# Kernel tuning notes

Measured on AMD Instinct MI355X. Metric: run time of the kernel, lower is better.

Reference implementation:

```python
import jax, jax.numpy as jnp
import numpy as np

DIM, HEAD, FFN = 256, 4, 1024
NEG = -1e9


def layer_norm(x, g, b, eps=1e-5):
    mu = jnp.mean(x, axis=-1, keepdims=True)
    var = jnp.mean((x - mu) ** 2, axis=-1, keepdims=True)
    return (x - mu) / jnp.sqrt(var + eps) * g + b


def setup_inputs() -> dict:
    key = jax.random.key(0)
    ks = jax.random.split(key, 10)
    B, T, D = 8, 2048, DIM
    s = 1.0 / np.sqrt(D)
    x = jax.random.normal(ks[0], (B, T, D), dtype=jnp.float32)
    mask = jax.random.randint(ks[1], (B, T), 0, 2).astype(jnp.float32)
    Wqkv = jax.random.uniform(ks[2], (3 * D, D), jnp.float32, -s, s)
    bqkv = jnp.zeros((3 * D,), jnp.float32)
    Wo = jax.random.uniform(ks[3], (D, D), jnp.float32, -s, s)
    bo = jnp.zeros((D,), jnp.float32)
    W1 = jax.random.uniform(ks[4], (FFN, D), jnp.float32, -s, s)
    b1 = jnp.zeros((FFN,), jnp.float32)
    W2 = jax.random.uniform(ks[5], (D, FFN), jnp.float32, -1.0 / np.sqrt(FFN), 1.0 / np.sqrt(FFN))
    b2 = jnp.zeros((D,), jnp.float32)
    g1 = jnp.ones((D,), jnp.float32); be1 = jnp.zeros((D,), jnp.float32)
    g2 = jnp.ones((D,), jnp.float32); be2 = jnp.zeros((D,), jnp.float32)
    return dict(x=x, mask=mask, Wqkv=Wqkv, bqkv=bqkv, Wo=Wo, bo=bo,
                W1=W1, b1=b1, W2=W2, b2=b2, g1=g1, be1=be1, g2=g2, be2=be2)


def _forward(x, mask, Wqkv, bqkv, Wo, bo, W1, b1, W2, b2, g1, be1, g2, be2):
    B, T, D = x.shape
    H = HEAD
    hd = D // H
    # --- MultiheadAttention (explicit, non-flash path, need_weights=True) ---
    qkv = jnp.einsum('btd,ed->bte', x, Wqkv) + bqkv            # (B,T,3D)
    q, k, v = jnp.split(qkv, 3, axis=-1)
    q = q.reshape(B, T, H, hd).transpose(0, 2, 1, 3)           # (B,H,T,hd)
    k = k.reshape(B, T, H, hd).transpose(0, 2, 1, 3)
    v = v.reshape(B, T, H, hd).transpose(0, 2, 1, 3)
    scores = jnp.einsum('bhqd,bhkd->bhqk', q, k) / jnp.sqrt(jnp.float32(hd))
    scores = jnp.where(mask[:, None, None, :] > 0.5, NEG, scores)
    w = jax.nn.softmax(scores, axis=-1)                        # (B,H,T,T)
    attn = jnp.einsum('bhqk,bhkd->bhqd', w, v)                 # (B,H,T,hd)
    attn = attn.transpose(0, 2, 1, 3).reshape(B, T, D)
    attn_out = jnp.einsum('btd,ed->bte', attn, Wo) + bo        # (B,T,D)
    w_avg = jnp.mean(w, axis=1)                                # (B,T,T), averaged over heads
    # halting score: sum over query dim (dim=1), then masked softmax
    halting = jnp.sum(w_avg, axis=1)                           # (B,T)
    halting = jax.nn.softmax(halting + mask * (-1e10), axis=-1)
    # --- residual + LN + FFN + LN ---
    h = layer_norm(x + attn_out, g1, be1)
    ffn = jnp.einsum('btf,df->btd', jax.nn.relu(jnp.einsum('btd,fd->btf', h, W1) + b1), W2) + b2
    out = layer_norm(h + ffn, g2, be2)
    return out, halting


def reference(x, mask, Wqkv, bqkv, Wo, bo, W1, b1, W2, b2, g1, be1, g2, be2):
    return _forward(x, mask, Wqkv, bqkv, Wo, bo, W1, b1, W2, b2, g1, be1, g2, be2)
```

## Files before the change

kernel.cpp:

```cpp
#include <hip/hip_runtime.h>
#include <hip/hip_bf16.h>
#include <math.h>

namespace {

constexpr int B = 8, T = 2048, D = 256, H = 4, HD = 64, FF = 1024;
constexpr float QSCALE = 0.18033688f;

typedef __attribute__((ext_vector_type(8))) short short8;
typedef __attribute__((ext_vector_type(4))) short s16x4;
typedef __attribute__((ext_vector_type(4))) float f32x4;

__device__ __forceinline__ float dot4(float4 a, float4 b) {
    return a.x*b.x + a.y*b.y + a.z*b.z + a.w*b.w;
}
__device__ __forceinline__ short f2bf(float f) {
    __hip_bfloat16 h = __float2bfloat16(f);
    return *reinterpret_cast<short*>(&h);
}
__device__ __forceinline__ float exp2a(float x) {
    float r; asm("v_exp_f32 %0, %1" : "=v"(r) : "v"(x)); return r;
}
__device__ __forceinline__ unsigned cvtpk(float lo, float hi) {
    unsigned r; asm("v_cvt_pk_bf16_f32 %0, %1, %2" : "=v"(r) : "v"(lo), "v"(hi)); return r;
}

__global__ __launch_bounds__(256) void k_cvt(
        const float* __restrict__ x,  const float* __restrict__ wq,
        const float* __restrict__ wo, const float* __restrict__ w1,
        const float* __restrict__ w2,
        short* __restrict__ x16,  short* __restrict__ wq16,
        short* __restrict__ wo16, short* __restrict__ w116,
        short* __restrict__ w216) {
    const int N0 = 524288, N1 = 24576, N2 = 8192, N3 = 32768, N4 = 32768;
    const int total = N0 + N1 + N2 + N3 + N4;
    for (int i = blockIdx.x*256 + threadIdx.x; i < total; i += gridDim.x*256) {
        const float* s; short* d; int j = i;
        if (j < N0) { s = x; d = x16; }
        else { j -= N0;
            if (j < N1) { s = wq; d = wq16; }
            else { j -= N1;
                if (j < N2) { s = wo; d = wo16; }
                else { j -= N2;
                    if (j < N3) { s = w1; d = w116; }
                    else { j -= N3; s = w2; d = w216; }
                }
            }
        }
        float4 a = ((const float4*)s)[j*2], b2 = ((const float4*)s)[j*2+1];
        short8 o;
        o[0]=f2bf(a.x);  o[1]=f2bf(a.y);  o[2]=f2bf(a.z);  o[3]=f2bf(a.w);
        o[4]=f2bf(b2.x); o[5]=f2bf(b2.y); o[6]=f2bf(b2.z); o[7]=f2bf(b2.w);
        ((short8*)d)[j] = o;
    }
}

template<int MODE>
__global__ __launch_bounds__(256) void k_gemm(
        const short* __restrict__ A, const short* __restrict__ W,
        const float* __restrict__ bias, const int K,
        short* __restrict__ oq, short* __restrict__ ok, short* __restrict__ ov,
        float* __restrict__ of, short* __restrict__ o16) {
    __shared__ short As[64][72];
    __shared__ short Ws[64][72];
    __shared__ float Cs[64][68];
    const int tid = threadIdx.x;
    const int w = tid >> 6, lane = tid & 63;
    const int qr = lane & 15, g = lane >> 4;
    const int wm = w >> 1, wn = w & 1;
    const int m0 = blockIdx.x * 64;
    const int n0 = blockIdx.y * 64;
    const int srow = tid >> 2, scol = (tid & 3) * 8;
    const short* Ag = A + (size_t)(m0 + srow) * K + scol;
    const short* Wg = W + (size_t)(n0 + srow) * K + scol;

    f32x4 acc[2][2];
    #pragma unroll
    for (int i = 0; i < 2; i++)
        #pragma unroll
        for (int j = 0; j < 2; j++) acc[i][j] = (f32x4){0.f, 0.f, 0.f, 0.f};

    for (int k0 = 0; k0 < K; k0 += 64) {
        __syncthreads();
        *(short8*)&As[srow][scol]      = *(const short8*)(Ag + k0);
        *(short8*)&As[srow][scol + 32] = *(const short8*)(Ag + k0 + 32);
        *(short8*)&Ws[srow][scol]      = *(const short8*)(Wg + k0);
        *(short8*)&Ws[srow][scol + 32] = *(const short8*)(Wg + k0 + 32);
        __syncthreads();
        #pragma unroll
        for (int kk = 0; kk < 2; kk++) {
            short8 a0 = *(const short8*)&As[wm*32 + qr][g*8 + kk*32];
            short8 a1 = *(const short8*)&As[wm*32 + 16 + qr][g*8 + kk*32];
            short8 b0 = *(const short8*)&Ws[wn*32 + qr][g*8 + kk*32];
            short8 b1 = *(const short8*)&Ws[wn*32 + 16 + qr][g*8 + kk*32];
            acc[0][0] = __builtin_amdgcn_mfma_f32_16x16x32_bf16(a0, b0, acc[0][0], 0, 0, 0);
            acc[0][1] = __builtin_amdgcn_mfma_f32_16x16x32_bf16(a0, b1, acc[0][1], 0, 0, 0);
            acc[1][0] = __builtin_amdgcn_mfma_f32_16x16x32_bf16(a1, b0, acc[1][0], 0, 0, 0);
            acc[1][1] = __builtin_amdgcn_mfma_f32_16x16x32_bf16(a1, b1, acc[1][1], 0, 0, 0);
        }
    }

    const int b = m0 >> 11;
    const int tl0 = m0 & (T - 1);

    if (MODE == 0 && blockIdx.y >= 8) {
        const int h = (int)blockIdx.y - 8;
        #pragma unroll
        for (int fm = 0; fm < 2; fm++) {
            const int tbase = tl0 + wm*32 + fm*16 + g*4;
            #pragma unroll
            for (int fn = 0; fn < 2; fn++) {
                const int d = wn*32 + fn*16 + qr;
                const float bv = bias[n0 + d];
                s16x4 pk;
                #pragma unroll
                for (int r = 0; r < 4; r++) pk[r] = f2bf(acc[fm][fn][r] + bv);
                *(s16x4*)&ov[((size_t)(b*H + h)*HD + d)*T + tbase] = pk;
            }
        }
        return;
    }

    #pragma unroll
    for (int fm = 0; fm < 2; fm++)
        #pragma unroll
        for (int fn = 0; fn < 2; fn++)
            #pragma unroll
            for (int r = 0; r < 4; r++)
                Cs[wm*32 + fm*16 + g*4 + r][wn*32 + fn*16 + qr] = acc[fm][fn][r];
    __syncthreads();
    const int row = tid >> 2, c0 = (tid & 3) * 16;
    float vals[16];
    #pragma unroll
    for (int j = 0; j < 16; j++) vals[j] = Cs[row][c0 + j] + bias[n0 + c0 + j];

    if (MODE == 0) {
        const int by = blockIdx.y;
        short* dst = (by < 4) ? oq : ok;
        const float qs = (by < 4) ? QSCALE : 1.0f;
        const int h = by & 3;
        short8 s0, s1;
        #pragma unroll
        for (int j = 0; j < 8; j++) { s0[j] = f2bf(vals[j]*qs); s1[j] = f2bf(vals[8+j]*qs); }
        short* p = dst + ((size_t)(b*H + h)*T + tl0 + row)*HD + c0;
        *(short8*)p = s0;
        *(short8*)(p + 8) = s1;
    } else if (MODE == 1 || MODE == 3) {
        float* p = of + (size_t)(m0 + row)*256 + n0 + c0;
        #pragma unroll
        for (int jj = 0; jj < 4; jj++) *(float4*)(p + jj*4) = *(float4*)&vals[jj*4];
    } else {
        short8 s0, s1;
        #pragma unroll
        for (int j = 0; j < 8; j++) {
            s0[j] = f2bf(fmaxf(vals[j], 0.f));
            s1[j] = f2bf(fmaxf(vals[8+j], 0.f));
        }
        short* p = o16 + (size_t)(m0 + row)*1024 + n0 + c0;
        *(short8*)p = s0;
        *(short8*)(p + 8) = s1;
    }
}

__global__ __launch_bounds__(256) void k_flash(
        const short* __restrict__ qb, const short* __restrict__ kb,
        const short* __restrict__ vtb, const float* __restrict__ mask,
        short* __restrict__ attnb, float* __restrict__ part) {
    __shared__ short Ks[64][72];
    __shared__ short Vt[64][72];
    __shared__ short Ps[4][16][72];
    __shared__ float msk[64];
    __shared__ float colacc[4][64];

    const int tid = threadIdx.x;
    const int w = tid >> 6, lane = tid & 63;
    const int qr = lane & 15, g = lane >> 4;
    const int qt = blockIdx.x, h = blockIdx.y, b = blockIdx.z;
    const int bh = b*H + h;
    const int q0 = qt*64 + w*16;

    const short* qg = qb + ((size_t)bh * T + q0) * HD;
    const short8 qf0 = *(const short8*)(qg + qr*HD + g*8);
    const short8 qf1 = *(const short8*)(qg + qr*HD + 32 + g*8);

    const short* kg0 = kb + (size_t)bh * T * HD;
    const short* vg0 = vtb + (size_t)bh * HD * T;
    const float* mg  = mask + (size_t)b * T;
    const int skey = tid >> 2, sc = tid & 3;

    float lrun = 0.f;
    f32x4 oa[4];
    #pragma unroll
    for (int i = 0; i < 4; i++) oa[i] = (f32x4){0.f, 0.f, 0.f, 0.f};

    for (int kt = 0; kt < T/64; kt++) {
        __syncthreads();
        {
            const short* kg = kg0 + (size_t)(kt*64) * HD;
            *(short8*)&Ks[skey][sc*8]      = *(const short8*)(kg + skey*HD + sc*8);
            *(short8*)&Ks[skey][sc*8 + 32] = *(const short8*)(kg + skey*HD + sc*8 + 32);
            const short* vg = vg0 + kt*64;
            *(short8*)&Vt[skey][sc*8]      = *(const short8*)(vg + (size_t)skey*T + sc*8);
            *(short8*)&Vt[skey][sc*8 + 32] = *(const short8*)(vg + (size_t)skey*T + sc*8 + 32);
            if (tid < 64) msk[tid] = mg[kt*64 + tid];
        }
        __syncthreads();

        float p[4][4];
        float lsum = 0.f;
        #pragma unroll
        for (int t4 = 0; t4 < 4; t4++) {
            f32x4 sa = (f32x4){0.f, 0.f, 0.f, 0.f};
            short8 kf0 = *(const short8*)&Ks[t4*16 + qr][g*8];
            short8 kf1 = *(const short8*)&Ks[t4*16 + qr][g*8 + 32];
            sa = __builtin_amdgcn_mfma_f32_16x16x32_bf16(kf0, qf0, sa, 0, 0, 0);
            sa = __builtin_amdgcn_mfma_f32_16x16x32_bf16(kf1, qf1, sa, 0, 0, 0);
            const float4 mv4 = *(const float4*)&msk[t4*16 + 4*g];
            p[t4][0] = (mv4.x > 0.5f) ? 0.f : exp2a(sa[0]);
            p[t4][1] = (mv4.y > 0.5f) ? 0.f : exp2a(sa[1]);
            p[t4][2] = (mv4.z > 0.5f) ? 0.f : exp2a(sa[2]);
            p[t4][3] = (mv4.w > 0.5f) ? 0.f : exp2a(sa[3]);
            lsum += (p[t4][0] + p[t4][1]) + (p[t4][2] + p[t4][3]);
        }
        lsum += __shfl_xor(lsum, 16, 64);
        lsum += __shfl_xor(lsum, 32, 64);
        lrun += lsum;

        #pragma unroll
        for (int t4 = 0; t4 < 4; t4++) {
            union { unsigned u[2]; s16x4 s; } cv;
            cv.u[0] = cvtpk(p[t4][0], p[t4][1]);
            cv.u[1] = cvtpk(p[t4][2], p[t4][3]);
            *(s16x4*)&Ps[w][qr][t4*16 + 4*g] = cv.s;
        }
        asm volatile("" ::: "memory");
        const short8 pa0 = *(const short8*)&Ps[w][qr][g*8];
        const short8 pa1 = *(const short8*)&Ps[w][qr][g*8 + 32];

        #pragma unroll
        for (int nt = 0; nt < 4; nt++) {
            short8 vf0 = *(const short8*)&Vt[nt*16 + qr][g*8];
            short8 vf1 = *(const short8*)&Vt[nt*16 + qr][g*8 + 32];
            oa[nt] = __builtin_amdgcn_mfma_f32_16x16x32_bf16(vf0, pa0, oa[nt], 0, 0, 0);
            oa[nt] = __builtin_amdgcn_mfma_f32_16x16x32_bf16(vf1, pa1, oa[nt], 0, 0, 0);
        }
    }

    const float invl = 1.f / lrun;
    #pragma unroll
    for (int nt = 0; nt < 4; nt++) {
        s16x4 pk;
        #pragma unroll
        for (int r = 0; r < 4; r++) pk[r] = f2bf(oa[nt][r] * invl);
        *(s16x4*)&attnb[((size_t)b*T + q0 + qr)*D + h*HD + nt*16 + 4*g] = pk;
    }
    float linv_r[4];
    #pragma unroll
    for (int r = 0; r < 4; r++) linv_r[r] = __shfl(invl, 4*g + r, 64);

    for (int kt = 0; kt < T/64; kt++) {
        __syncthreads();
        {
            const short* kg = kg0 + (size_t)(kt*64) * HD;
            *(short8*)&Ks[skey][sc*8]      = *(const short8*)(kg + skey*HD + sc*8);
            *(short8*)&Ks[skey][sc*8 + 32] = *(const short8*)(kg + skey*HD + sc*8 + 32);
            if (tid < 64) msk[tid] = mg[kt*64 + tid];
        }
        __syncthreads();
        float cs[4];
        #pragma unroll
        for (int t4 = 0; t4 < 4; t4++) {
            f32x4 sa = (f32x4){0.f, 0.f, 0.f, 0.f};
            short8 kf0 = *(const short8*)&Ks[t4*16 + qr][g*8];
            short8 kf1 = *(const short8*)&Ks[t4*16 + qr][g*8 + 32];
            sa = __builtin_amdgcn_mfma_f32_16x16x32_bf16(qf0, kf0, sa, 0, 0, 0);
            sa = __builtin_amdgcn_mfma_f32_16x16x32_bf16(qf1, kf1, sa, 0, 0, 0);
            float c = exp2a(sa[0])*linv_r[0] + exp2a(sa[1])*linv_r[1]
                    + exp2a(sa[2])*linv_r[2] + exp2a(sa[3])*linv_r[3];
            cs[t4] = (msk[t4*16 + qr] > 0.5f) ? 0.f : c;
        }
        #pragma unroll
        for (int t4 = 0; t4 < 4; t4++) {
            cs[t4] += __shfl_xor(cs[t4], 16, 64);
            cs[t4] += __shfl_xor(cs[t4], 32, 64);
        }
        if (lane < 16) {
            #pragma unroll
            for (int t4 = 0; t4 < 4; t4++) colacc[w][t4*16 + lane] = cs[t4];
        }
        __syncthreads();
        if (tid < 64)
            part[((size_t)bh*32 + qt)*T + kt*64 + tid] =
                colacc[0][tid] + colacc[1][tid] + colacc[2][tid] + colacc[3][tid];
    }
}

__global__ __launch_bounds__(256) void k_red(
        const float* __restrict__ part, float* __restrict__ red) {
    __shared__ float s[128];
    const int b = blockIdx.y, kc = blockIdx.x;
    const int tid = threadIdx.x;
    const int c = tid & 127, half = tid >> 7;
    const int k = kc*128 + c;
    const float* pb = part + ((size_t)(b*128 + half*64))*T + k;
    float acc = 0.f;
    #pragma unroll 8
    for (int r = 0; r < 64; r++) acc += pb[(size_t)r*T];
    if (half) s[c] = acc;
    __syncthreads();
    if (!half) red[(size_t)b*T + k] = acc + s[c];
}

__global__ __launch_bounds__(256) void k_halt(
        const float* __restrict__ red, const float* __restrict__ mask,
        float* __restrict__ outh) {
    __shared__ float redm[4], reds[4];
    const int b = blockIdx.x, tid = threadIdx.x;
    const float* mg = mask + (size_t)b * T;
    float v[8];
    float M = -3e38f;
    #pragma unroll
    for (int i = 0; i < 8; i++) {
        v[i] = red[(size_t)b*T + tid + i*256]*0.25f + mg[tid + i*256]*(-1e10f);
        M = fmaxf(M, v[i]);
    }
    #pragma unroll
    for (int off = 1; off < 64; off <<= 1) M = fmaxf(M, __shfl_xor(M, off, 64));
    const int wv = tid >> 6, lane = tid & 63;
    if (lane == 0) redm[wv] = M;
    __syncthreads();
    M = fmaxf(fmaxf(redm[0], redm[1]), fmaxf(redm[2], redm[3]));
    float S = 0.f;
    #pragma unroll
    for (int i = 0; i < 8; i++) { v[i] = __expf(v[i] - M); S += v[i]; }
    #pragma unroll
    for (int off = 1; off < 64; off <<= 1) S += __shfl_xor(S, off, 64);
    if (lane == 0) reds[wv] = S;
    __syncthreads();
    const float invS = 1.f / (reds[0] + reds[1] + reds[2] + reds[3]);
    #pragma unroll
    for (int i = 0; i < 8; i++) outh[(size_t)b*T + tid + i*256] = v[i]*invS;
}

__global__ __launch_bounds__(256) void k_ln(
        const float* __restrict__ a, const float* __restrict__ bsrc,
        const float* __restrict__ g, const float* __restrict__ be,
        float* __restrict__ yf, short* __restrict__ y16) {
    __shared__ float s[16][D];
    const int tid = threadIdx.x;
    const size_t row0 = (size_t)blockIdx.x * 16;
    const float4* ag = (const float4*)(a + row0*D);
    const float4* bg = (const float4*)(bsrc + row0*D);
    #pragma unroll
    for (int i = 0; i < 4; i++) {
        float4 av = ag[tid + i*256], bv = bg[tid + i*256];
        float4 sv = {av.x+bv.x, av.y+bv.y, av.z+bv.z, av.w+bv.w};
        ((float4*)&s[0][0])[tid + i*256] = sv;
    }
    __syncthreads();
    const int wv = tid >> 6, lane = tid & 63;
    float gvv[4], bvv[4];
    #pragma unroll
    for (int s2 = 0; s2 < 4; s2++) { gvv[s2] = g[lane + 64*s2]; bvv[s2] = be[lane + 64*s2]; }
    #pragma unroll
    for (int rr = 0; rr < 4; rr++) {
        const int r = wv*4 + rr;
        float x0 = s[r][lane],     x1 = s[r][lane+64];
        float x2 = s[r][lane+128], x3 = s[r][lane+192];
        float sum = x0+x1+x2+x3;
        float ssq = x0*x0 + x1*x1 + x2*x2 + x3*x3;
        #pragma unroll
        for (int off = 1; off < 64; off <<= 1) {
            sum += __shfl_xor(sum, off, 64);
            ssq += __shfl_xor(ssq, off, 64);
        }
        const float mu = sum * (1.f/256.f);
        const float rs = rsqrtf(ssq*(1.f/256.f) - mu*mu + 1e-5f);
        float y0 = (x0 - mu)*rs*gvv[0] + bvv[0];
        float y1 = (x1 - mu)*rs*gvv[1] + bvv[1];
        float y2 = (x2 - mu)*rs*gvv[2] + bvv[2];
        float y3 = (x3 - mu)*rs*gvv[3] + bvv[3];
        float* yp = yf + (row0 + r)*D;
        yp[lane]     = y0;
        yp[lane+64]  = y1;
        yp[lane+128] = y2;
        yp[lane+192] = y3;
        if (y16) {
            short* hp = y16 + (row0 + r)*D;
            hp[lane]     = f2bf(y0);
            hp[lane+64]  = f2bf(y1);
            hp[lane+128] = f2bf(y2);
            hp[lane+192] = f2bf(y3);
        }
    }
}

}

extern "C" void kernel_launch(void* const* d_in, const int* in_sizes, int n_in,
                              void* d_out, int out_size, void* d_ws, size_t ws_size,
                              hipStream_t stream) {
    (void)in_sizes; (void)n_in; (void)out_size; (void)ws_size;
    const float* x    = (const float*)d_in[0];
    const float* mask = (const float*)d_in[1];
    const float* Wqkv = (const float*)d_in[2];
    const float* bqkv = (const float*)d_in[3];
    const float* Wo   = (const float*)d_in[4];
    const float* bo   = (const float*)d_in[5];
    const float* W1   = (const float*)d_in[6];
    const float* b1   = (const float*)d_in[7];
    const float* W2   = (const float*)d_in[8];
    const float* b2   = (const float*)d_in[9];
    const float* g1   = (const float*)d_in[10];
    const float* be1  = (const float*)d_in[11];
    const float* g2   = (const float*)d_in[12];
    const float* be2  = (const float*)d_in[13];

    float* out  = (float*)d_out;
    char*  wsb  = (char*)d_ws;
    const size_t MB = 1024*1024;

    short* qb16   = (short*)(wsb + 0*MB);
    short* kb16   = (short*)(wsb + 8*MB);
    short* vt16   = (short*)(wsb + 16*MB);
    short* x16    = (short*)(wsb + 24*MB);
    short* attn16 = (short*)(wsb + 24*MB);
    float* part   = (float*)(wsb + 32*MB);
    float* hb     = (float*)(wsb + 40*MB);
    short* h16    = (short*)(wsb + 56*MB);
    short* wq16   = (short*)(wsb + 64*MB);
    short* wo16   = (short*)(wsb + 64*MB + 393216);
    short* w116   = (short*)(wsb + 64*MB + 524288);
    short* w216   = (short*)(wsb + 64*MB + 1048576);
    float* po     = (float*)(wsb + 66*MB);
    float* fo     = (float*)(wsb + 66*MB);
    short* mid16  = (short*)(wsb + 0*MB);
    float* redb   = (float*)(wsb + 82*MB);
    float* outh   = out + (size_t)B*T*D;

    k_cvt    <<<dim3(1024),        256, 0, stream>>>(x, Wqkv, Wo, W1, W2,
                                                     x16, wq16, wo16, w116, w216);
    k_gemm<0><<<dim3(256, 12),     256, 0, stream>>>(x16, wq16, bqkv, 256,
                                                     qb16, kb16, vt16, nullptr, nullptr);
    k_flash  <<<dim3(T/64, H, B),  256, 0, stream>>>(qb16, kb16, vt16, mask, attn16, part);
    k_red    <<<dim3(16, B),       256, 0, stream>>>(part, redb);
    k_halt   <<<dim3(B),           256, 0, stream>>>(redb, mask, outh);
    k_gemm<1><<<dim3(256, 4),      256, 0, stream>>>(attn16, wo16, bo, 256,
                                                     nullptr, nullptr, nullptr, po, nullptr);
    k_ln     <<<dim3(B*T/16),      256, 0, stream>>>(x, po, g1, be1, hb, h16);
    k_gemm<2><<<dim3(256, 16),     256, 0, stream>>>(h16, w116, b1, 256,
                                                     nullptr, nullptr, nullptr, nullptr, mid16);
    k_gemm<3><<<dim3(256, 4),      256, 0, stream>>>(mid16, w216, b2, 1024,
                                                     nullptr, nullptr, nullptr, fo, nullptr);
    k_ln     <<<dim3(B*T/16),      256, 0, stream>>>(hb, fo, g2, be2, out, nullptr);
}
```

Baseline: 241.3 us.

## Split attention kernel into key-split passes with a combine kernel

```diff
diff --git a/kernel.cpp b/kernel.cpp
--- a/kernel.cpp
+++ b/kernel.cpp
@@ -11,12 +11,14 @@
 typedef __attribute__((ext_vector_type(4))) short s16x4;
 typedef __attribute__((ext_vector_type(4))) float f32x4;
 
-__device__ __forceinline__ float dot4(float4 a, float4 b) {
-    return a.x*b.x + a.y*b.y + a.z*b.z + a.w*b.w;
-}
 __device__ __forceinline__ short f2bf(float f) {
     __hip_bfloat16 h = __float2bfloat16(f);
     return *reinterpret_cast<short*>(&h);
+}
+__device__ __forceinline__ float bf2f(short s) {
+    union { unsigned u; float f; } c;
+    c.u = ((unsigned)(unsigned short)s) << 16;
+    return c.f;
 }
 __device__ __forceinline__ float exp2a(float x) {
     float r; asm("v_exp_f32 %0, %1" : "=v"(r) : "v"(x)); return r;
@@ -162,20 +164,20 @@
     }
 }
 
-__global__ __launch_bounds__(256) void k_flash(
+__global__ __launch_bounds__(256) void k_flash1(
         const short* __restrict__ qb, const short* __restrict__ kb,
         const short* __restrict__ vtb, const float* __restrict__ mask,
-        short* __restrict__ attnb, float* __restrict__ part) {
+        short* __restrict__ opart, float* __restrict__ lpart) {
     __shared__ short Ks[64][72];
     __shared__ short Vt[64][72];
     __shared__ short Ps[4][16][72];
-    __shared__ float msk[64];
-    __shared__ float colacc[4][64];
+    __shared__ float mskb[64];
 
     const int tid = threadIdx.x;
     const int w = tid >> 6, lane = tid & 63;
     const int qr = lane & 15, g = lane >> 4;
-    const int qt = blockIdx.x, h = blockIdx.y, b = blockIdx.z;
+    const int kh = blockIdx.x & 1, qt = blockIdx.x >> 1;
+    const int h = blockIdx.y, b = blockIdx.z;
     const int bh = b*H + h;
     const int q0 = qt*64 + w*16;
 
@@ -183,9 +185,9 @@
     const short8 qf0 = *(const short8*)(qg + qr*HD + g*8);
     const short8 qf1 = *(const short8*)(qg + qr*HD + 32 + g*8);
 
-    const short* kg0 = kb + (size_t)bh * T * HD;
-    const short* vg0 = vtb + (size_t)bh * HD * T;
-    const float* mg  = mask + (size_t)b * T;
+    const short* kg0 = kb + (size_t)bh * T * HD + (size_t)kh * 1024 * HD;
+    const short* vg0 = vtb + (size_t)bh * HD * T + kh * 1024;
+    const float* mg  = mask + (size_t)b * T + kh * 1024;
     const int skey = tid >> 2, sc = tid & 3;
 
     float lrun = 0.f;
@@ -193,7 +195,7 @@
     #pragma unroll
     for (int i = 0; i < 4; i++) oa[i] = (f32x4){0.f, 0.f, 0.f, 0.f};
 
-    for (int kt = 0; kt < T/64; kt++) {
+    for (int kt = 0; kt < 16; kt++) {
         __syncthreads();
         {
             const short* kg = kg0 + (size_t)(kt*64) * HD;
@@ -202,7 +204,7 @@
             const short* vg = vg0 + kt*64;
             *(short8*)&Vt[skey][sc*8]      = *(const short8*)(vg + (size_t)skey*T + sc*8);
             *(short8*)&Vt[skey][sc*8 + 32] = *(const short8*)(vg + (size_t)skey*T + sc*8 + 32);
-            if (tid < 64) msk[tid] = mg[kt*64 + tid];
+            if (tid < 64) mskb[tid] = (mg[kt*64 + tid] > 0.5f) ? -1e9f : 0.f;
         }
         __syncthreads();
 
@@ -210,16 +212,16 @@
         float lsum = 0.f;
         #pragma unroll
         for (int t4 = 0; t4 < 4; t4++) {
-            f32x4 sa = (f32x4){0.f, 0.f, 0.f, 0.f};
+            const float4 mb4 = *(const float4*)&mskb[t4*16 + 4*g];
+            f32x4 sa = (f32x4){mb4.x, mb4.y, mb4.z, mb4.w};
             short8 kf0 = *(const short8*)&Ks[t4*16 + qr][g*8];
             short8 kf1 = *(const short8*)&Ks[t4*16 + qr][g*8 + 32];
             sa = __builtin_amdgcn_mfma_f32_16x16x32_bf16(kf0, qf0, sa, 0, 0, 0);
             sa = __builtin_amdgcn_mfma_f32_16x16x32_bf16(kf1, qf1, sa, 0, 0, 0);
-            const float4 mv4 = *(const float4*)&msk[t4*16 + 4*g];
-            p[t4][0] = (mv4.x > 0.5f) ? 0.f : exp2a(sa[0]);
-            p[t4][1] = (mv4.y > 0.5f) ? 0.f : exp2a(sa[1]);
-            p[t4][2] = (mv4.z > 0.5f) ? 0.f : exp2a(sa[2]);
-            p[t4][3] = (mv4.w > 0.5f) ? 0.f : exp2a(sa[3]);
+            p[t4][0] = exp2a(sa[0]);
+            p[t4][1] = exp2a(sa[1]);
+            p[t4][2] = exp2a(sa[2]);
+            p[t4][3] = exp2a(sa[3]);
             lsum += (p[t4][0] + p[t4][1]) + (p[t4][2] + p[t4][3]);
         }
         lsum += __shfl_xor(lsum, 16, 64);
@@ -246,38 +248,86 @@
         }
     }
 
-    const float invl = 1.f / lrun;
+    const size_t obase = ((size_t)(kh*32 + bh)*2048 + q0 + qr) * 64;
     #pragma unroll
     for (int nt = 0; nt < 4; nt++) {
         s16x4 pk;
         #pragma unroll
-        for (int r = 0; r < 4; r++) pk[r] = f2bf(oa[nt][r] * invl);
-        *(s16x4*)&attnb[((size_t)b*T + q0 + qr)*D + h*HD + nt*16 + 4*g] = pk;
-    }
-    float linv_r[4];
-    #pragma unroll
-    for (int r = 0; r < 4; r++) linv_r[r] = __shfl(invl, 4*g + r, 64);
-
-    for (int kt = 0; kt < T/64; kt++) {
+        for (int r = 0; r < 4; r++) pk[r] = f2bf(oa[nt][r]);
+        *(s16x4*)&opart[obase + nt*16 + 4*g] = pk;
+    }
+    if (lane < 16)
+        lpart[(size_t)(kh*32 + bh)*2048 + q0 + qr] = lrun;
+}
+
+__global__ __launch_bounds__(256) void k_comb(
+        const short* __restrict__ opart, const float* __restrict__ lpart,
+        short* __restrict__ attnb, float* __restrict__ invlb) {
+    const int j = blockIdx.x*256 + threadIdx.x;
+    const size_t flat = (size_t)j * 8;
+    const int d0 = (int)(flat & 63);
+    const int q  = (int)((flat >> 6) & 2047);
+    const int bh = (int)(flat >> 17);
+    short8 o0 = *(const short8*)&opart[flat];
+    short8 o1 = *(const short8*)&opart[flat + (size_t)4194304];
+    const float l = lpart[bh*2048 + q] + lpart[65536 + bh*2048 + q];
+    const float inv = 1.f / l;
+    short8 r;
+    #pragma unroll
+    for (int i = 0; i < 8; i++) r[i] = f2bf((bf2f(o0[i]) + bf2f(o1[i])) * inv);
+    const int b = bh >> 2, h = bh & 3;
+    *(short8*)&attnb[((size_t)(b*2048 + q))*256 + h*64 + d0] = r;
+    if (d0 == 0) invlb[bh*2048 + q] = inv;
+}
+
+__global__ __launch_bounds__(256) void k_flash2(
+        const short* __restrict__ qb, const short* __restrict__ kb,
+        const float* __restrict__ mask, const float* __restrict__ invlb,
+        float* __restrict__ part) {
+    __shared__ short Ks[64][72];
+    __shared__ float mskb[64];
+    __shared__ float colacc[4][64];
+
+    const int tid = threadIdx.x;
+    const int w = tid >> 6, lane = tid & 63;
+    const int qr = lane & 15, g = lane >> 4;
+    const int kh = blockIdx.x & 1, qt = blockIdx.x >> 1;
+    const int h = blockIdx.y, b = blockIdx.z;
+    const int bh = b*H + h;
+    const int q0 = qt*64 + w*16;
+
+    const short* qg = qb + ((size_t)bh * T + q0) * HD;
+    const short8 qf0 = *(const short8*)(qg + qr*HD + g*8);
+    const short8 qf1 = *(const short8*)(qg + qr*HD + 32 + g*8);
+
+    float linv[4];
+    #pragma unroll
+    for (int r = 0; r < 4; r++) linv[r] = invlb[bh*2048 + q0 + 4*g + r];
+
+    const short* kg0 = kb + (size_t)bh * T * HD + (size_t)kh * 1024 * HD;
+    const float* mg  = mask + (size_t)b * T + kh * 1024;
+    const int skey = tid >> 2, sc = tid & 3;
+
+    for (int kt = 0; kt < 16; kt++) {
         __syncthreads();
         {
             const short* kg = kg0 + (size_t)(kt*64) * HD;
             *(short8*)&Ks[skey][sc*8]      = *(const short8*)(kg + skey*HD + sc*8);
             *(short8*)&Ks[skey][sc*8 + 32] = *(const short8*)(kg + skey*HD + sc*8 + 32);
-            if (tid < 64) msk[tid] = mg[kt*64 + tid];
+            if (tid < 64) mskb[tid] = (mg[kt*64 + tid] > 0.5f) ? -1e9f : 0.f;
         }
         __syncthreads();
         float cs[4];
         #pragma unroll
         for (int t4 = 0; t4 < 4; t4++) {
-            f32x4 sa = (f32x4){0.f, 0.f, 0.f, 0.f};
+            const float mb = mskb[t4*16 + qr];
+            f32x4 sa = (f32x4){mb, mb, mb, mb};
             short8 kf0 = *(const short8*)&Ks[t4*16 + qr][g*8];
             short8 kf1 = *(const short8*)&Ks[t4*16 + qr][g*8 + 32];
             sa = __builtin_amdgcn_mfma_f32_16x16x32_bf16(qf0, kf0, sa, 0, 0, 0);
             sa = __builtin_amdgcn_mfma_f32_16x16x32_bf16(qf1, kf1, sa, 0, 0, 0);
-            float c = exp2a(sa[0])*linv_r[0] + exp2a(sa[1])*linv_r[1]
-                    + exp2a(sa[2])*linv_r[2] + exp2a(sa[3])*linv_r[3];
-            cs[t4] = (msk[t4*16 + qr] > 0.5f) ? 0.f : c;
+            cs[t4] = exp2a(sa[0])*linv[0] + exp2a(sa[1])*linv[1]
+                   + exp2a(sa[2])*linv[2] + exp2a(sa[3])*linv[3];
         }
         #pragma unroll
         for (int t4 = 0; t4 < 4; t4++) {
@@ -290,7 +340,7 @@
         }
         __syncthreads();
         if (tid < 64)
-            part[((size_t)bh*32 + qt)*T + kt*64 + tid] =
+            part[((size_t)bh*32 + qt)*T + kh*1024 + kt*64 + tid] =
                 colacc[0][tid] + colacc[1][tid] + colacc[2][tid] + colacc[3][tid];
     }
 }
@@ -425,24 +475,29 @@
     short* vt16   = (short*)(wsb + 16*MB);
     short* x16    = (short*)(wsb + 24*MB);
     short* attn16 = (short*)(wsb + 24*MB);
+    short* opart  = (short*)(wsb + 32*MB);
     float* part   = (float*)(wsb + 32*MB);
-    float* hb     = (float*)(wsb + 40*MB);
-    short* h16    = (short*)(wsb + 56*MB);
-    short* wq16   = (short*)(wsb + 64*MB);
-    short* wo16   = (short*)(wsb + 64*MB + 393216);
-    short* w116   = (short*)(wsb + 64*MB + 524288);
-    short* w216   = (short*)(wsb + 64*MB + 1048576);
-    float* po     = (float*)(wsb + 66*MB);
-    float* fo     = (float*)(wsb + 66*MB);
+    float* redb   = (float*)(wsb + 40*MB);
+    float* hb     = (float*)(wsb + 48*MB);
+    short* h16    = (short*)(wsb + 64*MB);
+    float* lpart  = (float*)(wsb + 72*MB);
+    float* invlb  = (float*)(wsb + 72*MB + 524288);
+    short* wq16   = (short*)(wsb + 73*MB);
+    short* wo16   = (short*)(wsb + 73*MB + 393216);
+    short* w116   = (short*)(wsb + 73*MB + 524288);
+    short* w216   = (short*)(wsb + 73*MB + 1048576);
+    float* po     = (float*)(wsb + 75*MB);
+    float* fo     = (float*)(wsb + 75*MB);
     short* mid16  = (short*)(wsb + 0*MB);
-    float* redb   = (float*)(wsb + 82*MB);
     float* outh   = out + (size_t)B*T*D;
 
     k_cvt    <<<dim3(1024),        256, 0, stream>>>(x, Wqkv, Wo, W1, W2,
                                                      x16, wq16, wo16, w116, w216);
     k_gemm<0><<<dim3(256, 12),     256, 0, stream>>>(x16, wq16, bqkv, 256,
                                                      qb16, kb16, vt16, nullptr, nullptr);
-    k_flash  <<<dim3(T/64, H, B),  256, 0, stream>>>(qb16, kb16, vt16, mask, attn16, part);
+    k_flash1 <<<dim3(64, H, B),    256, 0, stream>>>(qb16, kb16, vt16, mask, opart, lpart);
+    k_comb   <<<dim3(2048),        256, 0, stream>>>(opart, lpart, attn16, invlb);
+    k_flash2 <<<dim3(64, H, B),    256, 0, stream>>>(qb16, kb16, mask, invlb, part);
     k_red    <<<dim3(16, B),       256, 0, stream>>>(part, redb);
     k_halt   <<<dim3(B),           256, 0, stream>>>(redb, mask, outh);
     k_gemm<1><<<dim3(256, 4),      256, 0, stream>>>(attn16, wo16, bo, 256,
```

Result: no change. 237.6 us (-1.5%).

## Split flash attention into row-sum pass and fused normalized attention with column sums

Applied to the files above, without the earlier changes.

```diff
diff --git a/kernel.cpp b/kernel.cpp
--- a/kernel.cpp
+++ b/kernel.cpp
@@ -11,9 +11,6 @@
 typedef __attribute__((ext_vector_type(4))) short s16x4;
 typedef __attribute__((ext_vector_type(4))) float f32x4;
 
-__device__ __forceinline__ float dot4(float4 a, float4 b) {
-    return a.x*b.x + a.y*b.y + a.z*b.z + a.w*b.w;
-}
 __device__ __forceinline__ short f2bf(float f) {
     __hip_bfloat16 h = __float2bfloat16(f);
     return *reinterpret_cast<short*>(&h);
@@ -162,136 +159,227 @@
     }
 }
 
-__global__ __launch_bounds__(256) void k_flash(
+__global__ __launch_bounds__(256) void k_flashL(
         const short* __restrict__ qb, const short* __restrict__ kb,
-        const short* __restrict__ vtb, const float* __restrict__ mask,
-        short* __restrict__ attnb, float* __restrict__ part) {
-    __shared__ short Ks[64][72];
-    __shared__ short Vt[64][72];
-    __shared__ short Ps[4][16][72];
-    __shared__ float msk[64];
-    __shared__ float colacc[4][64];
-
+        const float* __restrict__ mask, float* __restrict__ liout) {
+    __shared__ short Ks[128][72];
+    __shared__ float lbuf[4][4][16];
     const int tid = threadIdx.x;
     const int w = tid >> 6, lane = tid & 63;
     const int qr = lane & 15, g = lane >> 4;
     const int qt = blockIdx.x, h = blockIdx.y, b = blockIdx.z;
     const int bh = b*H + h;
-    const int q0 = qt*64 + w*16;
-
-    const short* qg = qb + ((size_t)bh * T + q0) * HD;
-    const short8 qf0 = *(const short8*)(qg + qr*HD + g*8);
-    const short8 qf1 = *(const short8*)(qg + qr*HD + 32 + g*8);
-
+    const int q0 = qt*64;
+
+    short8 qf[4][2];
+    {
+        const short* qg = qb + ((size_t)bh * T + q0) * HD;
+        #pragma unroll
+        for (int qt4 = 0; qt4 < 4; qt4++) {
+            qf[qt4][0] = *(const short8*)(qg + (qt4*16 + qr)*HD + g*8);
+            qf[qt4][1] = *(const short8*)(qg + (qt4*16 + qr)*HD + 32 + g*8);
+        }
+    }
+    const short* kg0 = kb + (size_t)bh * T * HD;
+    const float* mg  = mask + (size_t)b * T;
+    const int krow = lane >> 1, khalf = (lane & 1) * 32;
+
+    float lrun[4] = {0.f, 0.f, 0.f, 0.f};
+
+    for (int kt = 0; kt < 16; kt++) {
+        const int kbase = kt*128 + w*32;
+        {
+            const short* ksrc = kg0 + (size_t)(kbase + krow)*HD + khalf;
+            short* kdst = &Ks[w*32 + krow][khalf];
+            #pragma unroll
+            for (int c = 0; c < 4; c++)
+                *(short8*)(kdst + c*8) = *(const short8*)(ksrc + c*8);
+        }
+        asm volatile("" ::: "memory");
+        #pragma unroll
+        for (int kt2 = 0; kt2 < 2; kt2++) {
+            short8 kf0 = *(const short8*)&Ks[w*32 + kt2*16 + qr][g*8];
+            short8 kf1 = *(const short8*)&Ks[w*32 + kt2*16 + qr][g*8 + 32];
+            const int key0 = kbase + kt2*16;
+            const float4 mv4 = *(const float4*)(mg + key0 + 4*g);
+            const float b0 = (mv4.x > 0.5f) ? -1e9f : 0.f;
+            const float b1 = (mv4.y > 0.5f) ? -1e9f : 0.f;
+            const float b2v = (mv4.z > 0.5f) ? -1e9f : 0.f;
+            const float b3 = (mv4.w > 0.5f) ? -1e9f : 0.f;
+            #pragma unroll
+            for (int qt4 = 0; qt4 < 4; qt4++) {
+                f32x4 sa = (f32x4){b0, b1, b2v, b3};
+                sa = __builtin_amdgcn_mfma_f32_16x16x32_bf16(kf0, qf[qt4][0], sa, 0, 0, 0);
+                sa = __builtin_amdgcn_mfma_f32_16x16x32_bf16(kf1, qf[qt4][1], sa, 0, 0, 0);
+                lrun[qt4] += (exp2a(sa[0]) + exp2a(sa[1])) + (exp2a(sa[2]) + exp2a(sa[3]));
+            }
+        }
+        asm volatile("" ::: "memory");
+    }
+    #pragma unroll
+    for (int qt4 = 0; qt4 < 4; qt4++) {
+        lrun[qt4] += __shfl_xor(lrun[qt4], 16, 64);
+        lrun[qt4] += __shfl_xor(lrun[qt4], 32, 64);
+    }
+    if (g == 0) {
+        #pragma unroll
+        for (int qt4 = 0; qt4 < 4; qt4++) lbuf[w][qt4][qr] = lrun[qt4];
+    }
+    __syncthreads();
+    if (tid < 64) {
+        const int qt4 = tid >> 4, qrr = tid & 15;
+        const float l = lbuf[0][qt4][qrr] + lbuf[1][qt4][qrr]
+                      + lbuf[2][qt4][qrr] + lbuf[3][qt4][qrr];
+        liout[(size_t)bh*T + q0 + tid] = -__log2f(l);
+    }
+}
+
+__global__ __launch_bounds__(256) void k_fattn(
+        const short* __restrict__ qb, const short* __restrict__ kb,
+        const short* __restrict__ vtb, const float* __restrict__ mask,
+        const float* __restrict__ liout,
+        short* __restrict__ attnb, float* __restrict__ part4) {
+    __shared__ short Ks[128][72];
+    __shared__ short Vt[64][136];
+    __shared__ short Ps[4][64][40];
+    const int tid = threadIdx.x;
+    const int w = tid >> 6, lane = tid & 63;
+    const int qr = lane & 15, g = lane >> 4;
+    const int qt = blockIdx.x, h = blockIdx.y, b = blockIdx.z;
+    const int bh = b*H + h;
+    const int q0 = qt*64;
+
+    short8 qf[4][2];
+    float li[4];
+    {
+        const short* qg = qb + ((size_t)bh * T + q0) * HD;
+        #pragma unroll
+        for (int qt4 = 0; qt4 < 4; qt4++) {
+            qf[qt4][0] = *(const short8*)(qg + (qt4*16 + qr)*HD + g*8);
+            qf[qt4][1] = *(const short8*)(qg + (qt4*16 + qr)*HD + 32 + g*8);
+            li[qt4] = liout[(size_t)bh*T + q0 + qt4*16 + qr];
+        }
+    }
     const short* kg0 = kb + (size_t)bh * T * HD;
     const short* vg0 = vtb + (size_t)bh * HD * T;
     const float* mg  = mask + (size_t)b * T;
-    const int skey = tid >> 2, sc = tid & 3;
-
-    float lrun = 0.f;
-    f32x4 oa[4];
-    #pragma unroll
-    for (int i = 0; i < 4; i++) oa[i] = (f32x4){0.f, 0.f, 0.f, 0.f};
-
-    for (int kt = 0; kt < T/64; kt++) {
+    float* csrow = part4 + (size_t)(bh*32 + qt) * T;
+    const int krow = lane >> 1, khalf = (lane & 1) * 32;
+
+    f32x4 oa[4][4];
+    #pragma unroll
+    for (int nt = 0; nt < 4; nt++)
+        #pragma unroll
+        for (int qt4 = 0; qt4 < 4; qt4++) oa[nt][qt4] = (f32x4){0.f,0.f,0.f,0.f};
+
+    short8 kreg[4], vreg[4];
+    #pragma unroll
+    for (int c = 0; c < 4; c++) {
+        kreg[c] = *(const short8*)(kg0 + (size_t)(w*32 + krow)*HD + khalf + c*8);
+        vreg[c] = *(const short8*)(vg0 + (size_t)lane*T + w*32 + c*8);
+    }
+    #pragma unroll
+    for (int c = 0; c < 4; c++) {
+        *(short8*)&Ks[w*32 + krow][khalf + c*8] = kreg[c];
+        *(short8*)&Vt[lane][w*32 + c*8] = vreg[c];
+    }
+    asm volatile("" ::: "memory");
+
+    for (int kt = 0; kt < 16; kt++) {
+        if (kt < 15) {
+            const int nb = (kt+1)*128 + w*32;
+            #pragma unroll
+            for (int c = 0; c < 4; c++) {
+                kreg[c] = *(const short8*)(kg0 + (size_t)(nb + krow)*HD + khalf + c*8);
+                vreg[c] = *(const short8*)(vg0 + (size_t)lane*T + nb + c*8);
+            }
+        }
+        const int kbase = kt*128 + w*32;
+        #pragma unroll
+        for (int kt2 = 0; kt2 < 2; kt2++) {
+            short8 kf0 = *(const short8*)&Ks[w*32 + kt2*16 + qr][g*8];
+            short8 kf1 = *(const short8*)&Ks[w*32 + kt2*16 + qr][g*8 + 32];
+            const int key0 = kbase + kt2*16;
+            const float4 mv4 = *(const float4*)(mg + key0 + 4*g);
+            const float mb[4] = { (mv4.x > 0.5f) ? -1e9f : 0.f,
+                                  (mv4.y > 0.5f) ? -1e9f : 0.f,
+                                  (mv4.z > 0.5f) ? -1e9f : 0.f,
+                                  (mv4.w > 0.5f) ? -1e9f : 0.f };
+            float p[4][4];
+            #pragma unroll
+            for (int qt4 = 0; qt4 < 4; qt4++) {
+                f32x4 sa = (f32x4){mb[0] + li[qt4], mb[1] + li[qt4],
+                                   mb[2] + li[qt4], mb[3] + li[qt4]};
+                sa = __builtin_amdgcn_mfma_f32_16x16x32_bf16(kf0, qf[qt4][0], sa, 0, 0, 0);
+                sa = __builtin_amdgcn_mfma_f32_16x16x32_bf16(kf1, qf[qt4][1], sa, 0, 0, 0);
+                p[qt4][0] = exp2a(sa[0]); p[qt4][1] = exp2a(sa[1]);
+                p[qt4][2] = exp2a(sa[2]); p[qt4][3] = exp2a(sa[3]);
+            }
+            float cs[4];
+            #pragma unroll
+            for (int r = 0; r < 4; r++) {
+                cs[r] = (p[0][r] + p[1][r]) + (p[2][r] + p[3][r]);
+                cs[r] += __shfl_xor(cs[r], 1, 64);
+                cs[r] += __shfl_xor(cs[r], 2, 64);
+                cs[r] += __shfl_xor(cs[r], 4, 64);
+                cs[r] += __shfl_xor(cs[r], 8, 64);
+            }
+            if (qr == 0) {
+                #pragma unroll
+                for (int r = 0; r < 4; r++) csrow[key0 + 4*g + r] = cs[r];
+            }
+            #pragma unroll
+            for (int qt4 = 0; qt4 < 4; qt4++) {
+                union { unsigned u[2]; s16x4 s; } cv;
+                cv.u[0] = cvtpk(p[qt4][0], p[qt4][1]);
+                cv.u[1] = cvtpk(p[qt4][2], p[qt4][3]);
+                *(s16x4*)&Ps[w][qt4*16 + qr][kt2*16 + 4*g] = cv.s;
+            }
+        }
+        asm volatile("" ::: "memory");
+        short8 pa[4];
+        #pragma unroll
+        for (int qt4 = 0; qt4 < 4; qt4++)
+            pa[qt4] = *(const short8*)&Ps[w][qt4*16 + qr][g*8];
+        #pragma unroll
+        for (int nt = 0; nt < 4; nt++) {
+            short8 vf = *(const short8*)&Vt[nt*16 + qr][w*32 + g*8];
+            #pragma unroll
+            for (int qt4 = 0; qt4 < 4; qt4++)
+                oa[nt][qt4] = __builtin_amdgcn_mfma_f32_16x16x32_bf16(vf, pa[qt4], oa[nt][qt4], 0, 0, 0);
+        }
+        if (kt < 15) {
+            asm volatile("" ::: "memory");
+            #pragma unroll
+            for (int c = 0; c < 4; c++) {
+                *(short8*)&Ks[w*32 + krow][khalf + c*8] = kreg[c];
+                *(short8*)&Vt[lane][w*32 + c*8] = vreg[c];
+            }
+            asm volatile("" ::: "memory");
+        }
+    }
+
+    __syncthreads();
+    float* Obuf = (float*)&Ks[0][0];
+    const int qL = tid >> 2, dq = tid & 3;
+    #pragma unroll
+    for (int nt = 0; nt < 4; nt++) {
+        #pragma unroll
+        for (int qt4 = 0; qt4 < 4; qt4++)
+            #pragma unroll
+            for (int r = 0; r < 4; r++)
+                Obuf[(w*16 + 4*g + r)*68 + qt4*16 + qr] = oa[nt][qt4][r];
         __syncthreads();
-        {
-            const short* kg = kg0 + (size_t)(kt*64) * HD;
-            *(short8*)&Ks[skey][sc*8]      = *(const short8*)(kg + skey*HD + sc*8);
-            *(short8*)&Ks[skey][sc*8 + 32] = *(const short8*)(kg + skey*HD + sc*8 + 32);
-            const short* vg = vg0 + kt*64;
-            *(short8*)&Vt[skey][sc*8]      = *(const short8*)(vg + (size_t)skey*T + sc*8);
-            *(short8*)&Vt[skey][sc*8 + 32] = *(const short8*)(vg + (size_t)skey*T + sc*8 + 32);
-            if (tid < 64) msk[tid] = mg[kt*64 + tid];
-        }
+        s16x4 pk;
+        #pragma unroll
+        for (int rr = 0; rr < 4; rr++) {
+            const int dr = dq*4 + rr;
+            float v = Obuf[(0*16 + dr)*68 + qL] + Obuf[(1*16 + dr)*68 + qL]
+                    + Obuf[(2*16 + dr)*68 + qL] + Obuf[(3*16 + dr)*68 + qL];
+            pk[rr] = f2bf(v);
+        }
+        *(s16x4*)&attnb[((size_t)b*T + q0 + qL)*D + h*HD + nt*16 + dq*4] = pk;
         __syncthreads();
-
-        float p[4][4];
-        float lsum = 0.f;
-        #pragma unroll
-        for (int t4 = 0; t4 < 4; t4++) {
-            f32x4 sa = (f32x4){0.f, 0.f, 0.f, 0.f};
-            short8 kf0 = *(const short8*)&Ks[t4*16 + qr][g*8];
-            short8 kf1 = *(const short8*)&Ks[t4*16 + qr][g*8 + 32];
-            sa = __builtin_amdgcn_mfma_f32_16x16x32_bf16(kf0, qf0, sa, 0, 0, 0);
-            sa = __builtin_amdgcn_mfma_f32_16x16x32_bf16(kf1, qf1, sa, 0, 0, 0);
-            const float4 mv4 = *(const float4*)&msk[t4*16 + 4*g];
-            p[t4][0] = (mv4.x > 0.5f) ? 0.f : exp2a(sa[0]);
-            p[t4][1] = (mv4.y > 0.5f) ? 0.f : exp2a(sa[1]);
-            p[t4][2] = (mv4.z > 0.5f) ? 0.f : exp2a(sa[2]);
-            p[t4][3] = (mv4.w > 0.5f) ? 0.f : exp2a(sa[3]);
-            lsum += (p[t4][0] + p[t4][1]) + (p[t4][2] + p[t4][3]);
-        }
-        lsum += __shfl_xor(lsum, 16, 64);
-        lsum += __shfl_xor(lsum, 32, 64);
-        lrun += lsum;
-
-        #pragma unroll
-        for (int t4 = 0; t4 < 4; t4++) {
-            union { unsigned u[2]; s16x4 s; } cv;
-            cv.u[0] = cvtpk(p[t4][0], p[t4][1]);
-            cv.u[1] = cvtpk(p[t4][2], p[t4][3]);
-            *(s16x4*)&Ps[w][qr][t4*16 + 4*g] = cv.s;
-        }
-        asm volatile("" ::: "memory");
-        const short8 pa0 = *(const short8*)&Ps[w][qr][g*8];
-        const short8 pa1 = *(const short8*)&Ps[w][qr][g*8 + 32];
-
-        #pragma unroll
-        for (int nt = 0; nt < 4; nt++) {
-            short8 vf0 = *(const short8*)&Vt[nt*16 + qr][g*8];
-            short8 vf1 = *(const short8*)&Vt[nt*16 + qr][g*8 + 32];
-            oa[nt] = __builtin_amdgcn_mfma_f32_16x16x32_bf16(vf0, pa0, oa[nt], 0, 0, 0);
-            oa[nt] = __builtin_amdgcn_mfma_f32_16x16x32_bf16(vf1, pa1, oa[nt], 0, 0, 0);
-        }
-    }
-
-    const float invl = 1.f / lrun;
-    #pragma unroll
-    for (int nt = 0; nt < 4; nt++) {
-        s16x4 pk;
-        #pragma unroll
-        for (int r = 0; r < 4; r++) pk[r] = f2bf(oa[nt][r] * invl);
-        *(s16x4*)&attnb[((size_t)b*T + q0 + qr)*D + h*HD + nt*16 + 4*g] = pk;
-    }
-    float linv_r[4];
-    #pragma unroll
-    for (int r = 0; r < 4; r++) linv_r[r] = __shfl(invl, 4*g + r, 64);
-
-    for (int kt = 0; kt < T/64; kt++) {
-        __syncthreads();
-        {
-            const short* kg = kg0 + (size_t)(kt*64) * HD;
-            *(short8*)&Ks[skey][sc*8]      = *(const short8*)(kg + skey*HD + sc*8);
-            *(short8*)&Ks[skey][sc*8 + 32] = *(const short8*)(kg + skey*HD + sc*8 + 32);
-            if (tid < 64) msk[tid] = mg[kt*64 + tid];
-        }
-        __syncthreads();
-        float cs[4];
-        #pragma unroll
-        for (int t4 = 0; t4 < 4; t4++) {
-            f32x4 sa = (f32x4){0.f, 0.f, 0.f, 0.f};
-            short8 kf0 = *(const short8*)&Ks[t4*16 + qr][g*8];
-            short8 kf1 = *(const short8*)&Ks[t4*16 + qr][g*8 + 32];
-            sa = __builtin_amdgcn_mfma_f32_16x16x32_bf16(qf0, kf0, sa, 0, 0, 0);
-            sa = __builtin_amdgcn_mfma_f32_16x16x32_bf16(qf1, kf1, sa, 0, 0, 0);
-            float c = exp2a(sa[0])*linv_r[0] + exp2a(sa[1])*linv_r[1]
-                    + exp2a(sa[2])*linv_r[2] + exp2a(sa[3])*linv_r[3];
-            cs[t4] = (msk[t4*16 + qr] > 0.5f) ? 0.f : c;
-        }
-        #pragma unroll
-        for (int t4 = 0; t4 < 4; t4++) {
-            cs[t4] += __shfl_xor(cs[t4], 16, 64);
-            cs[t4] += __shfl_xor(cs[t4], 32, 64);
-        }
-        if (lane < 16) {
-            #pragma unroll
-            for (int t4 = 0; t4 < 4; t4++) colacc[w][t4*16 + lane] = cs[t4];
-        }
-        __syncthreads();
-        if (tid < 64)
-            part[((size_t)bh*32 + qt)*T + kt*64 + tid] =
-                colacc[0][tid] + colacc[1][tid] + colacc[2][tid] + colacc[3][tid];
     }
 }
 
@@ -425,25 +513,28 @@
     short* vt16   = (short*)(wsb + 16*MB);
     short* x16    = (short*)(wsb + 24*MB);
     short* attn16 = (short*)(wsb + 24*MB);
-    float* part   = (float*)(wsb + 32*MB);
-    float* hb     = (float*)(wsb + 40*MB);
-    short* h16    = (short*)(wsb + 56*MB);
-    short* wq16   = (short*)(wsb + 64*MB);
-    short* wo16   = (short*)(wsb + 64*MB + 393216);
-    short* w116   = (short*)(wsb + 64*MB + 524288);
-    short* w216   = (short*)(wsb + 64*MB + 1048576);
-    float* po     = (float*)(wsb + 66*MB);
-    float* fo     = (float*)(wsb + 66*MB);
     short* mid16  = (short*)(wsb + 0*MB);
-    float* redb   = (float*)(wsb + 82*MB);
+    float* part4  = (float*)(wsb + 32*MB);
+    float* redb   = (float*)(wsb + 40*MB);
+    float* liout  = (float*)(wsb + 41*MB);
+    short* wq16   = (short*)(wsb + 42*MB);
+    short* wo16   = (short*)(wsb + 42*MB + 393216);
+    short* w116   = (short*)(wsb + 42*MB + 524288);
+    short* w216   = (short*)(wsb + 42*MB + 1048576);
+    float* hb     = (float*)(wsb + 44*MB);
+    short* h16    = (short*)(wsb + 60*MB);
+    float* po     = (float*)(wsb + 68*MB);
+    float* fo     = (float*)(wsb + 68*MB);
     float* outh   = out + (size_t)B*T*D;
 
     k_cvt    <<<dim3(1024),        256, 0, stream>>>(x, Wqkv, Wo, W1, W2,
                                                      x16, wq16, wo16, w116, w216);
     k_gemm<0><<<dim3(256, 12),     256, 0, stream>>>(x16, wq16, bqkv, 256,
                                                      qb16, kb16, vt16, nullptr, nullptr);
-    k_flash  <<<dim3(T/64, H, B),  256, 0, stream>>>(qb16, kb16, vt16, mask, attn16, part);
-    k_red    <<<dim3(16, B),       256, 0, stream>>>(part, redb);
+    k_flashL <<<dim3(32, H, B),    256, 0, stream>>>(qb16, kb16, mask, liout);
+    k_fattn  <<<dim3(32, H, B),    256, 0, stream>>>(qb16, kb16, vt16, mask, liout,
+                                                     attn16, part4);
+    k_red    <<<dim3(16, B),       256, 0, stream>>>(part4, redb);
     k_halt   <<<dim3(B),           256, 0, stream>>>(redb, mask, outh);
     k_gemm<1><<<dim3(256, 4),      256, 0, stream>>>(attn16, wo16, bo, 256,
                                                      nullptr, nullptr, nullptr, po, nullptr);
```

Result: faster. 230.6 us (-4.5%).
